# Kernel tuning notes

Measured on AMD Instinct MI355X. Metric: run time of the kernel, lower is better.

## Reference

```python
import jax, jax.numpy as jnp
import numpy as np

B, S, N, P = 16, 1, 6, 70000
H0, W0, DS = 448, 800, 4
H, W = H0 // DS, W0 // DS          # 112, 200
BEV_SIDE = 200


def _apply_4x4(RT, xyz):
    # RT: [M,4,4], xyz: [M,P,3] -> [M,P,3]
    xyz1 = jnp.concatenate([xyz, jnp.ones_like(xyz[..., :1])], axis=-1)
    return jnp.einsum('mij,mpj->mpi', RT, xyz1)[..., :3]


def _scale_intrinsics4(K, sx, sy):
    # K: [M,3,3] pinhole intrinsics -> scaled, embedded in 4x4
    M = K.shape[0]
    K4 = jnp.tile(jnp.eye(4, dtype=K.dtype), (M, 1, 1))
    K4 = K4.at[:, 0, 0].set(K[:, 0, 0] * sx)
    K4 = K4.at[:, 1, 1].set(K[:, 1, 1] * sy)
    K4 = K4.at[:, 0, 2].set(K[:, 0, 2] * sx)
    K4 = K4.at[:, 1, 2].set(K[:, 1, 2] * sy)
    return K4


def setup_inputs() -> dict:
    rng = np.random.default_rng(0)
    pts = rng.uniform(-50.0, 50.0, size=(B, 1, 1, P, 3)).astype(np.float32)
    pts[..., 2] = rng.uniform(-2.0, 4.0, size=(B, 1, 1, P)).astype(np.float32)
    ilu = rng.uniform(0.0, 255.0, size=(B, 1, 1, P, 1)).astype(np.float32)
    pcloud = np.concatenate([pts, ilu], axis=-1)
    # extrinsics: cam-to-car pose, 6 cameras at yaw 0..300deg
    E = np.tile(np.eye(4, dtype=np.float32), (B, S, N, 1, 1))
    for n in range(N):
        a = 2.0 * np.pi * n / N
        c, s = np.cos(a), np.sin(a)
        E[:, :, n, :3, :3] = np.array([[c, -s, 0], [s, c, 0], [0, 0, 1]], np.float32)
        E[:, :, n, :3, 3] = np.array([2.0 * c, 2.0 * s, 1.5], np.float32)
    K = np.tile(np.eye(3, dtype=np.float32), (B, S, N, 1, 1))
    K[..., 0, 0] = 500.0
    K[..., 1, 1] = 500.0
    K[..., 0, 2] = W0 / 2.0
    K[..., 1, 2] = H0 / 2.0
    V = np.tile(np.eye(4, dtype=np.float32), (B, 1, 1, 1, 1))
    V[..., 0, 0] = 2.0
    V[..., 1, 1] = 2.0
    V[..., 0, 3] = 100.0
    V[..., 1, 3] = 100.0
    return {
        'pcloud': jnp.asarray(pcloud),
        'extrinsics': jnp.asarray(E),
        'intrinsics': jnp.asarray(K),
        'view': jnp.asarray(V),
        'bev_side': BEV_SIDE,
    }


def reference(pcloud, extrinsics, intrinsics, view, bev_side):
    sx = sy = 1.0 / DS
    bsn = B * S * N
    lidar_coords = pcloud[:, 0, 0, :, :3]                      # [B,P,3]
    ilu = jnp.repeat(pcloud[:, 0, 0, :, 3], N, axis=0)         # [BSN,P]
    view2 = view[:, 0, 0]                                      # [B,4,4]
    lidar_view = _apply_4x4(jnp.linalg.inv(view2), lidar_coords)
    xyz_car = jnp.repeat(lidar_view, N, axis=0)                # [BSN,P,3]
    K = intrinsics.reshape(bsn, 3, 3)
    E = extrinsics.reshape(bsn, 4, 4)
    Rt = jnp.swapaxes(E[:, :3, :3], 1, 2)
    Einv = E.at[:, :3, :3].set(Rt).at[:, :3, 3:4].set(-jnp.matmul(Rt, E[:, :3, 3:4]))
    pixel_from_car = jnp.matmul(_scale_intrinsics4(K, sx, sy), Einv)
    z = _apply_4x4(Einv, xyz_car)[:, :, 2]                     # cam-frame depth
    xyz_pixel = _apply_4x4(pixel_from_car, xyz_car)            # [BSN,P,3]
    normalizer = xyz_pixel[:, :, 2]
    xy = xyz_pixel[:, :, :2] / jnp.maximum(normalizer[..., None], 1e-6)
    x_, y_ = xy[:, :, 0], xy[:, :, 1]
    valid = ((x_ > -0.5) & (x_ < W - 0.5) & (y_ > -0.5) & (y_ < H - 0.5) & (z > 0.0)).astype(pcloud.dtype)
    depth = jnp.clip(normalizer, 0.0, bev_side / 2 - 1) * valid
    vilu = jnp.clip(ilu * valid, 0.0, 255.0)
    ym = jnp.clip(y_, 0.0, H - 1).astype(jnp.int32)
    xm = jnp.clip(x_, 0.0, W - 1).astype(jnp.int32)
    b = jnp.broadcast_to(jnp.arange(bsn)[:, None], (bsn, P))
    depth_grid = jnp.zeros((bsn, H, W), pcloud.dtype).at[b, ym, xm].set(depth)
    ilu_grid = jnp.zeros((bsn, H, W), pcloud.dtype).at[b, ym, xm].set(vilu)
    ilu_grid = jnp.log1p(ilu_grid) / np.log(256.0)
    depth_grid = depth_grid / (bev_side / 2)
    return jnp.concatenate([depth_grid[:, None], ilu_grid[:, None]], axis=1)  # [BSN,2,H,W]
```

## Files before the change

### kernel.cpp

```cpp
#include <hip/hip_runtime.h>
#include <math.h>

#define B_    16
#define N_    6
#define P_    70000
#define H_    112
#define W_    200
#define HW_   (H_ * W_)
#define BSN_  (B_ * N_)
#define HALF_ 56
#define CELLS_ (HALF_ * W_)
#define NSEG  4
#define SEGPTS (P_ / NSEG)
#define T1_   512
#define T2_   1024

#define WS_NEED ((size_t)BSN_ * 2 * NSEG * CELLS_ * 4)


__device__ __forceinline__ float rdot4(float r0, float r1, float r2, float r3,
                                       float x, float y, float z) {
    float s = r0 * x;
    s = fmaf(r1, y, s);
    s = fmaf(r2, z, s);
    return s + r3;
}

__device__ __forceinline__ void inv4(const float* m, float* o) {
    float inv[16];
    inv[0]  =  m[5]*m[10]*m[15] - m[5]*m[11]*m[14] - m[9]*m[6]*m[15] + m[9]*m[7]*m[14] + m[13]*m[6]*m[11] - m[13]*m[7]*m[10];
    inv[4]  = -m[4]*m[10]*m[15] + m[4]*m[11]*m[14] + m[8]*m[6]*m[15] - m[8]*m[7]*m[14] - m[12]*m[6]*m[11] + m[12]*m[7]*m[10];
    inv[8]  =  m[4]*m[9]*m[15]  - m[4]*m[11]*m[13] - m[8]*m[5]*m[15] + m[8]*m[7]*m[13] + m[12]*m[5]*m[11] - m[12]*m[7]*m[9];
    inv[12] = -m[4]*m[9]*m[14]  + m[4]*m[10]*m[13] + m[8]*m[5]*m[14] - m[8]*m[6]*m[13] - m[12]*m[5]*m[10] + m[12]*m[6]*m[9];
    inv[1]  = -m[1]*m[10]*m[15] + m[1]*m[11]*m[14] + m[9]*m[2]*m[15] - m[9]*m[3]*m[14] - m[13]*m[2]*m[11] + m[13]*m[3]*m[10];
    inv[5]  =  m[0]*m[10]*m[15] - m[0]*m[11]*m[14] - m[8]*m[2]*m[15] + m[8]*m[3]*m[14] + m[12]*m[2]*m[11] - m[12]*m[3]*m[10];
    inv[9]  = -m[0]*m[9]*m[15]  + m[0]*m[11]*m[13] + m[8]*m[1]*m[15] - m[8]*m[3]*m[13] - m[12]*m[1]*m[11] + m[12]*m[3]*m[9];
    inv[13] =  m[0]*m[9]*m[14]  - m[0]*m[10]*m[13] - m[8]*m[1]*m[14] + m[8]*m[2]*m[13] + m[12]*m[1]*m[10] - m[12]*m[2]*m[9];
    inv[2]  =  m[1]*m[6]*m[15]  - m[1]*m[7]*m[14]  - m[5]*m[2]*m[15] + m[5]*m[3]*m[14] + m[13]*m[2]*m[7]  - m[13]*m[3]*m[6];
    inv[6]  = -m[0]*m[6]*m[15]  + m[0]*m[7]*m[14]  + m[4]*m[2]*m[15] - m[4]*m[3]*m[14] - m[12]*m[2]*m[7]  + m[12]*m[3]*m[6];
    inv[10] =  m[0]*m[5]*m[15]  - m[0]*m[7]*m[13]  - m[4]*m[1]*m[15] + m[4]*m[3]*m[13] + m[12]*m[1]*m[7]  - m[12]*m[3]*m[5];
    inv[14] = -m[0]*m[5]*m[14]  + m[0]*m[6]*m[13]  + m[4]*m[1]*m[14] - m[4]*m[2]*m[13] - m[12]*m[1]*m[6]  + m[12]*m[2]*m[5];
    inv[3]  = -m[1]*m[6]*m[11]  + m[1]*m[7]*m[10]  + m[5]*m[2]*m[11] - m[5]*m[3]*m[10] - m[9]*m[2]*m[7]   + m[9]*m[3]*m[6];
    inv[7]  =  m[0]*m[6]*m[11]  - m[0]*m[7]*m[10]  - m[4]*m[2]*m[11] + m[4]*m[3]*m[10] + m[8]*m[2]*m[7]   - m[8]*m[3]*m[6];
    inv[11] = -m[0]*m[5]*m[11]  + m[0]*m[7]*m[9]   + m[4]*m[1]*m[11] - m[4]*m[3]*m[9]  - m[8]*m[1]*m[7]   + m[8]*m[3]*m[5];
    inv[15] =  m[0]*m[5]*m[10]  - m[0]*m[6]*m[9]   - m[4]*m[1]*m[10] + m[4]*m[2]*m[9]  + m[8]*m[1]*m[6]   - m[8]*m[2]*m[5];
    float det = m[0]*inv[0] + m[1]*inv[4] + m[2]*inv[8] + m[3]*inv[12];
    float rdet = 1.0f / det;
    for (int i = 0; i < 16; ++i) o[i] = inv[i] * rdet;
}

__device__ __forceinline__ void cam_mats(const float* Ein, const float* Kin,
                                         float E2[4], float PFC[3][4]) {
    float Einv[4][4];
    for (int i = 0; i < 3; ++i)
        for (int j = 0; j < 3; ++j)
            Einv[i][j] = Ein[j * 4 + i];
    for (int i = 0; i < 3; ++i) {
        float s = Ein[0 * 4 + i] * Ein[0 * 4 + 3];
        s = fmaf(Ein[1 * 4 + i], Ein[1 * 4 + 3], s);
        s = fmaf(Ein[2 * 4 + i], Ein[2 * 4 + 3], s);
        Einv[i][3] = -s;
    }
    Einv[3][0] = Ein[12]; Einv[3][1] = Ein[13];
    Einv[3][2] = Ein[14]; Einv[3][3] = Ein[15];

    float K4[4][4] = {};
    K4[0][0] = Kin[0] * 0.25f;  K4[0][2] = Kin[2] * 0.25f;
    K4[1][1] = Kin[4] * 0.25f;  K4[1][2] = Kin[5] * 0.25f;
    K4[2][2] = 1.0f;            K4[3][3] = 1.0f;

    for (int i = 0; i < 3; ++i)
        for (int j = 0; j < 4; ++j) {
            float s = K4[i][0] * Einv[0][j];
            s = fmaf(K4[i][1], Einv[1][j], s);
            s = fmaf(K4[i][2], Einv[2][j], s);
            s = fmaf(K4[i][3], Einv[3][j], s);
            PFC[i][j] = s;
        }
    for (int j = 0; j < 4; ++j) E2[j] = Einv[2][j];
}


__global__ __launch_bounds__(T1_) void k_partial(
        const float4* __restrict__ pc, const float* __restrict__ extr,
        const float* __restrict__ intr, const float* __restrict__ view,
        int* __restrict__ partial) {
    __shared__ int   win[CELLS_];
    __shared__ float sM[24];

    const int i    = blockIdx.x;
    const int xcd  = i & 7;
    const int j    = i >> 3;
    const int b    = xcd + 8 * (j >= 48 ? 1 : 0);
    const int r    = j % 48;
    const int cam  = r >> 3;
    const int half = (r >> 2) & 1;
    const int seg  = r & 3;
    const int m    = b * N_ + cam;
    const int rlo  = half * HALF_;
    const int t    = threadIdx.x;

    if (t == 0) {
        float Vi[16];
        inv4(&view[b * 16], Vi);
        for (int k = 0; k < 12; ++k) sM[k] = Vi[k];
    } else if (t == 64) {
        float E2[4], PFC[3][4];
        cam_mats(&extr[m * 16], &intr[m * 9], E2, PFC);
        for (int ii = 0; ii < 3; ++ii)
            for (int jj = 0; jj < 4; ++jj) sM[12 + ii * 4 + jj] = PFC[ii][jj];
    }
    for (int k = t; k < CELLS_; k += T1_) win[k] = -1;
    __syncthreads();

    const float V0 = sM[0],  V1 = sM[1],  V2 = sM[2],  V3 = sM[3];
    const float V4 = sM[4],  V5 = sM[5],  V6 = sM[6],  V7 = sM[7];
    const float V8 = sM[8],  V9 = sM[9],  V10 = sM[10], V11 = sM[11];
    const float P00 = sM[12], P01 = sM[13], P02 = sM[14], P03 = sM[15];
    const float P10 = sM[16], P11 = sM[17], P12 = sM[18], P13 = sM[19];
    const float P20 = sM[20], P21 = sM[21], P22 = sM[22], P23 = sM[23];

    const float4* pcb = pc + (size_t)b * P_;
    int c0 = -1, c1 = -1, c2 = -1, c3 = -1;
    const int p0 = seg * SEGPTS;

    for (int p = p0 + t; p < p0 + SEGPTS; p += T1_) {
        float4 pt = pcb[p];
        float lx = rdot4(V0, V1, V2,  V3,  pt.x, pt.y, pt.z);
        float ly = rdot4(V4, V5, V6,  V7,  pt.x, pt.y, pt.z);
        float lz = rdot4(V8, V9, V10, V11, pt.x, pt.y, pt.z);
        float px = rdot4(P00, P01, P02, P03, lx, ly, lz);
        float py = rdot4(P10, P11, P12, P13, lx, ly, lz);
        float pz = rdot4(P20, P21, P22, P23, lx, ly, lz);
        float denom = fmaxf(pz, 1e-6f);
        float x_ = px / denom;
        float y_ = py / denom;
        int ym = (int)fminf(fmaxf(y_, 0.0f), (float)(H_ - 1));
        int xm = (int)fminf(fmaxf(x_, 0.0f), (float)(W_ - 1));
        bool is_c = (xm == 0 || xm == W_ - 1) && (ym == 0 || ym == H_ - 1);
        int code = ((ym != 0) << 1) | (xm != 0);
        c0 = (is_c && code == 0) ? p : c0;
        c1 = (is_c && code == 1) ? p : c1;
        c2 = (is_c && code == 2) ? p : c2;
        c3 = (is_c && code == 3) ? p : c3;
        int rr = ym - rlo;
        if (!is_c && (unsigned)rr < (unsigned)HALF_)
            atomicMax(&win[rr * W_ + xm], p);
    }
    for (int d = 32; d; d >>= 1) {
        c0 = max(c0, __shfl_xor(c0, d));
        c1 = max(c1, __shfl_xor(c1, d));
        c2 = max(c2, __shfl_xor(c2, d));
        c3 = max(c3, __shfl_xor(c3, d));
    }
    if ((t & 63) == 0) {
        if (half == 0) {
            if (c0 >= 0) atomicMax(&win[0],   c0);
            if (c1 >= 0) atomicMax(&win[199], c1);
        } else {
            if (c2 >= 0) atomicMax(&win[(H_ - 1 - rlo) * W_ + 0],   c2);
            if (c3 >= 0) atomicMax(&win[(H_ - 1 - rlo) * W_ + 199], c3);
        }
    }
    __syncthreads();

    int* dst = partial + (size_t)(((m * 2 + half) * NSEG) + seg) * CELLS_;
    for (int k = t; k < CELLS_; k += T1_) dst[k] = win[k];
}


__global__ __launch_bounds__(T2_) void k_mergefin(
        const float4* __restrict__ pc, const int* __restrict__ partial,
        const float* __restrict__ extr, const float* __restrict__ intr,
        const float* __restrict__ view,
        float* __restrict__ out, const int* __restrict__ bev_side_p) {
    __shared__ float sM[28];

    const int i    = blockIdx.x;
    const int xcd  = i & 7;
    const int j    = i >> 3;
    const int b    = xcd + 8 * (j >= 12 ? 1 : 0);
    const int r    = j % 12;
    const int cam  = r >> 1;
    const int half = r & 1;
    const int m    = b * N_ + cam;
    const int rlo  = half * HALF_;
    const int t    = threadIdx.x;

    if (t == 0) {
        float Vi[16];
        inv4(&view[b * 16], Vi);
        for (int k = 0; k < 12; ++k) sM[k] = Vi[k];
    } else if (t == 64) {
        float E2[4], PFC[3][4];
        cam_mats(&extr[m * 16], &intr[m * 9], E2, PFC);
        for (int ii = 0; ii < 3; ++ii)
            for (int jj = 0; jj < 4; ++jj) sM[12 + ii * 4 + jj] = PFC[ii][jj];
        for (int jj = 0; jj < 4; ++jj) sM[24 + jj] = E2[jj];
    }
    __syncthreads();

    const float bev_half = (float)bev_side_p[0] * 0.5f;
    const float clip_hi  = bev_half - 1.0f;
    const float4* pcb = pc + (size_t)b * P_;
    const int* pp = partial + (size_t)((m * 2 + half) * NSEG) * CELLS_;
    const int base0 = (m * 2) * HW_ + rlo * W_;

    for (int rr = t; rr < CELLS_; rr += T2_) {
        int wv = max(max(pp[rr], pp[CELLS_ + rr]),
                     max(pp[2 * CELLS_ + rr], pp[3 * CELLS_ + rr]));
        float depth = 0.0f, iluv = 0.0f;
        if (wv >= 0) {
            float4 pt = pcb[wv];
            float lx = rdot4(sM[0],  sM[1],  sM[2],  sM[3],  pt.x, pt.y, pt.z);
            float ly = rdot4(sM[4],  sM[5],  sM[6],  sM[7],  pt.x, pt.y, pt.z);
            float lz = rdot4(sM[8],  sM[9],  sM[10], sM[11], pt.x, pt.y, pt.z);
            float z  = rdot4(sM[24], sM[25], sM[26], sM[27], lx, ly, lz);
            float px = rdot4(sM[12], sM[13], sM[14], sM[15], lx, ly, lz);
            float py = rdot4(sM[16], sM[17], sM[18], sM[19], lx, ly, lz);
            float pz = rdot4(sM[20], sM[21], sM[22], sM[23], lx, ly, lz);
            float denom = fmaxf(pz, 1e-6f);
            float x_ = px / denom;
            float y_ = py / denom;
            bool valid = (x_ > -0.5f) && (x_ < (float)W_ - 0.5f) &&
                         (y_ > -0.5f) && (y_ < (float)H_ - 0.5f) && (z > 0.0f);
            if (valid) {
                float d = fminf(fmaxf(pz, 0.0f), clip_hi);
                depth = d / bev_half;
                float vi = fminf(fmaxf(pt.w, 0.0f), 255.0f);
                iluv = log1pf(vi) / 5.545177444479562f;
            }
        }
        out[base0 + rr]       = depth;
        out[base0 + HW_ + rr] = iluv;
    }
}


#define PMAIN 69632
#define PTAIL (P_ - PMAIN)

__global__ __launch_bounds__(1024, 4) void k_lidar_ilp(
        const float4* __restrict__ pc, const float* __restrict__ extr,
        const float* __restrict__ intr, const float* __restrict__ view,
        float* __restrict__ out, const int* __restrict__ bev_side_p) {
    __shared__ int   win[CELLS_];
    __shared__ float sM[28];

    const int i    = blockIdx.x;
    const int xcd  = i & 7;
    const int s    = i >> 3;
    const int b    = xcd + 8 * (s >= 12 ? 1 : 0);
    const int c12  = s % 12;
    const int m    = b * N_ + (c12 >> 1);
    const int rlo  = (c12 & 1) * HALF_;
    const int t    = threadIdx.x;

    if (t == 0) {
        float Vi[16];
        inv4(&view[b * 16], Vi);
        for (int k = 0; k < 12; ++k) sM[k] = Vi[k];
    } else if (t == 64) {
        float E2[4], PFC[3][4];
        cam_mats(&extr[m * 16], &intr[m * 9], E2, PFC);
        for (int ii = 0; ii < 3; ++ii)
            for (int jj = 0; jj < 4; ++jj) sM[12 + ii * 4 + jj] = PFC[ii][jj];
        for (int jj = 0; jj < 4; ++jj) sM[24 + jj] = E2[jj];
    }
    for (int k = t; k < CELLS_; k += 1024) win[k] = -1;
    __syncthreads();

    const float V0 = sM[0],  V1 = sM[1],  V2 = sM[2],  V3 = sM[3];
    const float V4 = sM[4],  V5 = sM[5],  V6 = sM[6],  V7 = sM[7];
    const float V8 = sM[8],  V9 = sM[9],  V10 = sM[10], V11 = sM[11];
    const float P00 = sM[12], P01 = sM[13], P02 = sM[14], P03 = sM[15];
    const float P10 = sM[16], P11 = sM[17], P12 = sM[18], P13 = sM[19];
    const float P20 = sM[20], P21 = sM[21], P22 = sM[22], P23 = sM[23];

    const float4* pcb = pc + (size_t)b * P_;
    int c0 = -1, c1 = -1, c2 = -1, c3 = -1;

#define PROC(PT, PIDX)                                                        \
    {                                                                         \
        float lx = rdot4(V0, V1, V2,  V3,  (PT).x, (PT).y, (PT).z);           \
        float ly = rdot4(V4, V5, V6,  V7,  (PT).x, (PT).y, (PT).z);           \
        float lz = rdot4(V8, V9, V10, V11, (PT).x, (PT).y, (PT).z);           \
        float px = rdot4(P00, P01, P02, P03, lx, ly, lz);                     \
        float py = rdot4(P10, P11, P12, P13, lx, ly, lz);                     \
        float pz = rdot4(P20, P21, P22, P23, lx, ly, lz);                     \
        float denom = fmaxf(pz, 1e-6f);                                       \
        float x_ = px / denom;                                                \
        float y_ = py / denom;                                                \
        int ym = (int)fminf(fmaxf(y_, 0.0f), (float)(H_ - 1));                \
        int xm = (int)fminf(fmaxf(x_, 0.0f), (float)(W_ - 1));                \
        bool is_c = (xm == 0 || xm == W_ - 1) && (ym == 0 || ym == H_ - 1);   \
        int code = ((ym != 0) << 1) | (xm != 0);                              \
        c0 = (is_c && code == 0) ? (PIDX) : c0;                               \
        c1 = (is_c && code == 1) ? (PIDX) : c1;                               \
        c2 = (is_c && code == 2) ? (PIDX) : c2;                               \
        c3 = (is_c && code == 3) ? (PIDX) : c3;                               \
        int rr = ym - rlo;                                                    \
        if (!is_c && (unsigned)rr < (unsigned)HALF_)                          \
            atomicMax(&win[rr * W_ + xm], (PIDX));                            \
    }

    for (int base = 0; base < PMAIN; base += 4 * 1024) {
        float4 q0 = pcb[base + t];
        float4 q1 = pcb[base + t + 1024];
        float4 q2 = pcb[base + t + 2 * 1024];
        float4 q3 = pcb[base + t + 3 * 1024];
        PROC(q0, base + t)
        PROC(q1, base + t + 1024)
        PROC(q2, base + t + 2 * 1024)
        PROC(q3, base + t + 3 * 1024)
    }
    if (t < PTAIL) {
        float4 q = pcb[PMAIN + t];
        PROC(q, PMAIN + t)
    }
#undef PROC

    for (int d = 32; d; d >>= 1) {
        c0 = max(c0, __shfl_xor(c0, d));
        c1 = max(c1, __shfl_xor(c1, d));
        c2 = max(c2, __shfl_xor(c2, d));
        c3 = max(c3, __shfl_xor(c3, d));
    }
    if ((t & 63) == 0) {
        if (rlo == 0) {
            if (c0 >= 0) atomicMax(&win[0],   c0);
            if (c1 >= 0) atomicMax(&win[199], c1);
        } else {
            if (c2 >= 0) atomicMax(&win[(H_ - 1 - rlo) * W_ + 0],   c2);
            if (c3 >= 0) atomicMax(&win[(H_ - 1 - rlo) * W_ + 199], c3);
        }
    }
    __syncthreads();

    const float bev_half = (float)bev_side_p[0] * 0.5f;
    const float clip_hi  = bev_half - 1.0f;
    const float E20 = sM[24], E21 = sM[25], E22 = sM[26], E23 = sM[27];
    const int base0 = (m * 2) * HW_ + rlo * W_;
    for (int r = t; r < CELLS_; r += 1024) {
        int w = win[r];
        float depth = 0.0f, iluv = 0.0f;
        if (w >= 0) {
            float4 pt = pcb[w];
            float lx = rdot4(V0, V1, V2,  V3,  pt.x, pt.y, pt.z);
            float ly = rdot4(V4, V5, V6,  V7,  pt.x, pt.y, pt.z);
            float lz = rdot4(V8, V9, V10, V11, pt.x, pt.y, pt.z);
            float z  = rdot4(E20, E21, E22, E23, lx, ly, lz);
            float px = rdot4(P00, P01, P02, P03, lx, ly, lz);
            float py = rdot4(P10, P11, P12, P13, lx, ly, lz);
            float pz = rdot4(P20, P21, P22, P23, lx, ly, lz);
            float denom = fmaxf(pz, 1e-6f);
            float x_ = px / denom;
            float y_ = py / denom;
            bool valid = (x_ > -0.5f) && (x_ < (float)W_ - 0.5f) &&
                         (y_ > -0.5f) && (y_ < (float)H_ - 0.5f) && (z > 0.0f);
            if (valid) {
                float d = fminf(fmaxf(pz, 0.0f), clip_hi);
                depth = d / bev_half;
                float vi = fminf(fmaxf(pt.w, 0.0f), 255.0f);
                iluv = log1pf(vi) / 5.545177444479562f;
            }
        }
        out[base0 + r]       = depth;
        out[base0 + HW_ + r] = iluv;
    }
}


extern "C" void kernel_launch(void* const* d_in, const int* in_sizes, int n_in,
                              void* d_out, int out_size, void* d_ws, size_t ws_size,
                              hipStream_t stream) {
    const float4* pc  = (const float4*)d_in[0];
    const float* extr = (const float*)d_in[1];
    const float* intr = (const float*)d_in[2];
    const float* view = (const float*)d_in[3];
    const int*   bev  = (const int*)d_in[4];
    float* out = (float*)d_out;

    if (ws_size >= WS_NEED) {
        int* partial = (int*)d_ws;
        k_partial<<<dim3(BSN_ * 2 * NSEG), dim3(T1_), 0, stream>>>(
            pc, extr, intr, view, partial);
        k_mergefin<<<dim3(BSN_ * 2), dim3(T2_), 0, stream>>>(
            pc, partial, extr, intr, view, out, bev);
    } else {
        k_lidar_ilp<<<dim3(BSN_ * 2), dim3(1024), 0, stream>>>(
            pc, extr, intr, view, out, bev);
    }
}
```

Baseline: 48.56 us.

## Replace per-camera partial grids with single-pass multi-camera scan and compacted hit lists

The first kernel now reads each lidar point once per batch, projects it into all six cameras, and uses division-free threshold tests to classify it. Only points that land strictly inside the image are appended, as packed (camera, cell, index) entries, to a per-block list in workspace; corner hits go to per-chunk reduction slots. The final kernel rebuilds each half-image winner map in shared memory from those compacted lists and corner maxima. This removes the redundant six-fold point reads and the large partial-grid writes and merges, at the cost of a shared-memory counter atomic per hit and of every final block scanning all entries of its batch.

```diff
diff --git a/kernel.cpp b/kernel.cpp
--- a/kernel.cpp
+++ b/kernel.cpp
@@ -10,12 +10,18 @@
 #define BSN_  (B_ * N_)
 #define HALF_ 56
 #define CELLS_ (HALF_ * W_)
-#define NSEG  4
-#define SEGPTS (P_ / NSEG)
-#define T1_   512
-#define T2_   1024
-
-#define WS_NEED ((size_t)BSN_ * 2 * NSEG * CELLS_ * 4)
+
+#define AT_     512
+#define AIT     8
+#define ACHUNK  (AT_ * AIT)
+#define ACHUNKS 18
+#define NBLK    (B_ * ACHUNKS)
+#define CAP     (ACHUNK * N_)
+
+#define WS_GC_OFF   0
+#define WS_CNT_OFF  (NBLK * 24 * 4)
+#define WS_ENT_OFF  32768
+#define WS_NEED     (WS_ENT_OFF + (size_t)NBLK * CAP * 8)
 
 
 __device__ __forceinline__ float rdot4(float r0, float r1, float r2, float r3,
@@ -81,108 +87,134 @@
 }
 
 
-__global__ __launch_bounds__(T1_) void k_partial(
+__global__ __launch_bounds__(AT_) void k_scan(
         const float4* __restrict__ pc, const float* __restrict__ extr,
         const float* __restrict__ intr, const float* __restrict__ view,
-        int* __restrict__ partial) {
-    __shared__ int   win[CELLS_];
-    __shared__ float sM[24];
-
-    const int i    = blockIdx.x;
-    const int xcd  = i & 7;
-    const int j    = i >> 3;
-    const int b    = xcd + 8 * (j >= 48 ? 1 : 0);
-    const int r    = j % 48;
-    const int cam  = r >> 3;
-    const int half = (r >> 2) & 1;
-    const int seg  = r & 3;
-    const int m    = b * N_ + cam;
-    const int rlo  = half * HALF_;
-    const int t    = threadIdx.x;
+        int* __restrict__ gcorner, int* __restrict__ counts,
+        uint2* __restrict__ entries) {
+    __shared__ float sM[84];
+    __shared__ int   swc[8][24];
+    __shared__ int   scnt;
+
+    const int b     = blockIdx.x;
+    const int chunk = blockIdx.y;
+    const int t     = threadIdx.x;
+    const int lane  = t & 63;
+    const int w     = t >> 6;
 
     if (t == 0) {
         float Vi[16];
         inv4(&view[b * 16], Vi);
         for (int k = 0; k < 12; ++k) sM[k] = Vi[k];
-    } else if (t == 64) {
+        scnt = 0;
+    } else if (t >= 64 && t < 64 + N_) {
+        int n = t - 64;
         float E2[4], PFC[3][4];
-        cam_mats(&extr[m * 16], &intr[m * 9], E2, PFC);
-        for (int ii = 0; ii < 3; ++ii)
-            for (int jj = 0; jj < 4; ++jj) sM[12 + ii * 4 + jj] = PFC[ii][jj];
-    }
-    for (int k = t; k < CELLS_; k += T1_) win[k] = -1;
-    __syncthreads();
-
-    const float V0 = sM[0],  V1 = sM[1],  V2 = sM[2],  V3 = sM[3];
-    const float V4 = sM[4],  V5 = sM[5],  V6 = sM[6],  V7 = sM[7];
-    const float V8 = sM[8],  V9 = sM[9],  V10 = sM[10], V11 = sM[11];
-    const float P00 = sM[12], P01 = sM[13], P02 = sM[14], P03 = sM[15];
-    const float P10 = sM[16], P11 = sM[17], P12 = sM[18], P13 = sM[19];
-    const float P20 = sM[20], P21 = sM[21], P22 = sM[22], P23 = sM[23];
-
+        cam_mats(&extr[(b * N_ + n) * 16], &intr[(b * N_ + n) * 9], E2, PFC);
+        for (int i = 0; i < 3; ++i)
+            for (int j = 0; j < 4; ++j) sM[12 + n * 12 + i * 4 + j] = PFC[i][j];
+    }
+    __syncthreads();
+
+    float V[12];
+    #pragma unroll
+    for (int k = 0; k < 12; ++k) V[k] = sM[k];
+    float Pm[6][12];
+    #pragma unroll
+    for (int n = 0; n < 6; ++n)
+        #pragma unroll
+        for (int k = 0; k < 12; ++k) Pm[n][k] = sM[12 + n * 12 + k];
+
+    int c[24];
+    #pragma unroll
+    for (int k = 0; k < 24; ++k) c[k] = -1;
+
+    const int blk = b * ACHUNKS + chunk;
+    uint2* ent = entries + (size_t)blk * CAP;
     const float4* pcb = pc + (size_t)b * P_;
-    int c0 = -1, c1 = -1, c2 = -1, c3 = -1;
-    const int p0 = seg * SEGPTS;
-
-    for (int p = p0 + t; p < p0 + SEGPTS; p += T1_) {
-        float4 pt = pcb[p];
-        float lx = rdot4(V0, V1, V2,  V3,  pt.x, pt.y, pt.z);
-        float ly = rdot4(V4, V5, V6,  V7,  pt.x, pt.y, pt.z);
-        float lz = rdot4(V8, V9, V10, V11, pt.x, pt.y, pt.z);
-        float px = rdot4(P00, P01, P02, P03, lx, ly, lz);
-        float py = rdot4(P10, P11, P12, P13, lx, ly, lz);
-        float pz = rdot4(P20, P21, P22, P23, lx, ly, lz);
-        float denom = fmaxf(pz, 1e-6f);
-        float x_ = px / denom;
-        float y_ = py / denom;
-        int ym = (int)fminf(fmaxf(y_, 0.0f), (float)(H_ - 1));
-        int xm = (int)fminf(fmaxf(x_, 0.0f), (float)(W_ - 1));
-        bool is_c = (xm == 0 || xm == W_ - 1) && (ym == 0 || ym == H_ - 1);
-        int code = ((ym != 0) << 1) | (xm != 0);
-        c0 = (is_c && code == 0) ? p : c0;
-        c1 = (is_c && code == 1) ? p : c1;
-        c2 = (is_c && code == 2) ? p : c2;
-        c3 = (is_c && code == 3) ? p : c3;
-        int rr = ym - rlo;
-        if (!is_c && (unsigned)rr < (unsigned)HALF_)
-            atomicMax(&win[rr * W_ + xm], p);
-    }
-    for (int d = 32; d; d >>= 1) {
-        c0 = max(c0, __shfl_xor(c0, d));
-        c1 = max(c1, __shfl_xor(c1, d));
-        c2 = max(c2, __shfl_xor(c2, d));
-        c3 = max(c3, __shfl_xor(c3, d));
-    }
-    if ((t & 63) == 0) {
-        if (half == 0) {
-            if (c0 >= 0) atomicMax(&win[0],   c0);
-            if (c1 >= 0) atomicMax(&win[199], c1);
-        } else {
-            if (c2 >= 0) atomicMax(&win[(H_ - 1 - rlo) * W_ + 0],   c2);
-            if (c3 >= 0) atomicMax(&win[(H_ - 1 - rlo) * W_ + 199], c3);
-        }
-    }
-    __syncthreads();
-
-    int* dst = partial + (size_t)(((m * 2 + half) * NSEG) + seg) * CELLS_;
-    for (int k = t; k < CELLS_; k += T1_) dst[k] = win[k];
-}
-
-
-__global__ __launch_bounds__(T2_) void k_mergefin(
-        const float4* __restrict__ pc, const int* __restrict__ partial,
-        const float* __restrict__ extr, const float* __restrict__ intr,
-        const float* __restrict__ view,
+
+    int p = chunk * ACHUNK + t;
+    for (int it = 0; it < AIT; ++it, p += AT_) {
+        bool valid = (p < P_);
+        float4 pt = make_float4(0.f, 0.f, 0.f, 0.f);
+        if (valid) pt = pcb[p];
+        float lx = rdot4(V[0], V[1], V[2],  V[3],  pt.x, pt.y, pt.z);
+        float ly = rdot4(V[4], V[5], V[6],  V[7],  pt.x, pt.y, pt.z);
+        float lz = rdot4(V[8], V[9], V[10], V[11], pt.x, pt.y, pt.z);
+        unsigned rfl = 0;
+        #pragma unroll
+        for (int n = 0; n < 6; ++n) {
+            float px = rdot4(Pm[n][0], Pm[n][1], Pm[n][2],  Pm[n][3],  lx, ly, lz);
+            float py = rdot4(Pm[n][4], Pm[n][5], Pm[n][6],  Pm[n][7],  lx, ly, lz);
+            float pz = rdot4(Pm[n][8], Pm[n][9], Pm[n][10], Pm[n][11], lx, ly, lz);
+            float denom = fmaxf(pz, 1e-6f);
+            float tl = 0.99f * denom;
+            float tx = 201.0f * denom;
+            float ty = 113.0f * denom;
+            bool x0 = (px <= tl), x1 = (px >= tx);
+            bool y0 = (py <= tl), y1 = (py >= ty);
+            if (valid) {
+                if (x0 & y0) c[n * 4 + 0] = p;
+                if (x1 & y0) c[n * 4 + 1] = p;
+                if (x0 & y1) c[n * 4 + 2] = p;
+                if (x1 & y1) c[n * 4 + 3] = p;
+                if (!((x0 | x1) & (y0 | y1))) rfl |= (1u << n);
+            }
+        }
+        if (__ballot(rfl != 0)) {
+            #pragma unroll
+            for (int n = 0; n < 6; ++n) {
+                if (rfl & (1u << n)) {
+                    float px = rdot4(Pm[n][0], Pm[n][1], Pm[n][2],  Pm[n][3],  lx, ly, lz);
+                    float py = rdot4(Pm[n][4], Pm[n][5], Pm[n][6],  Pm[n][7],  lx, ly, lz);
+                    float pz = rdot4(Pm[n][8], Pm[n][9], Pm[n][10], Pm[n][11], lx, ly, lz);
+                    float denom = fmaxf(pz, 1e-6f);
+                    float x_ = px / denom;
+                    float y_ = py / denom;
+                    int ym = (int)fminf(fmaxf(y_, 0.0f), (float)(H_ - 1));
+                    int xm = (int)fminf(fmaxf(x_, 0.0f), (float)(W_ - 1));
+                    int pos = atomicAdd(&scnt, 1);
+                    ent[pos] = make_uint2(((unsigned)n << 15) |
+                                          ((unsigned)ym << 8) | (unsigned)xm,
+                                          (unsigned)p);
+                }
+            }
+        }
+    }
+
+    #pragma unroll
+    for (int k = 0; k < 24; ++k) {
+        int v = c[k];
+        for (int d = 32; d; d >>= 1) v = max(v, __shfl_xor(v, d));
+        if (lane == 0) swc[w][k] = v;
+    }
+    __syncthreads();
+    if (t < 24) {
+        int v = -1;
+        #pragma unroll
+        for (int w2 = 0; w2 < 8; ++w2) v = max(v, swc[w2][t]);
+        gcorner[blk * 24 + t] = v;
+    }
+    if (t == 32) counts[blk] = scnt;
+}
+
+
+__global__ __launch_bounds__(1024) void k_fin(
+        const float4* __restrict__ pc, const float* __restrict__ extr,
+        const float* __restrict__ intr, const float* __restrict__ view,
+        const int* __restrict__ gcorner, const int* __restrict__ counts,
+        const uint2* __restrict__ entries,
         float* __restrict__ out, const int* __restrict__ bev_side_p) {
+    __shared__ int   win[CELLS_];
     __shared__ float sM[28];
 
     const int i    = blockIdx.x;
     const int xcd  = i & 7;
-    const int j    = i >> 3;
-    const int b    = xcd + 8 * (j >= 12 ? 1 : 0);
-    const int r    = j % 12;
-    const int cam  = r >> 1;
-    const int half = r & 1;
+    const int s    = i >> 3;
+    const int b    = xcd + 8 * (s >= 12 ? 1 : 0);
+    const int c12  = s % 12;
+    const int cam  = c12 >> 1;
+    const int half = c12 & 1;
     const int m    = b * N_ + cam;
     const int rlo  = half * HALF_;
     const int t    = threadIdx.x;
@@ -198,17 +230,41 @@
             for (int jj = 0; jj < 4; ++jj) sM[12 + ii * 4 + jj] = PFC[ii][jj];
         for (int jj = 0; jj < 4; ++jj) sM[24 + jj] = E2[jj];
     }
+    for (int k = t; k < CELLS_; k += 1024) win[k] = -1;
+    __syncthreads();
+
+    if (t < 2) {
+        int cid = half * 2 + t;
+        int best = -1;
+        for (int k = 0; k < ACHUNKS; ++k)
+            best = max(best, gcorner[(b * ACHUNKS + k) * 24 + cam * 4 + cid]);
+        if (best >= 0) {
+            int cell = (half ? (HALF_ - 1) * W_ : 0) + (t ? (W_ - 1) : 0);
+            atomicMax(&win[cell], best);
+        }
+    }
+
+    for (int k = 0; k < ACHUNKS; ++k) {
+        const int cnt = counts[b * ACHUNKS + k];
+        const uint2* ent = entries + (size_t)(b * ACHUNKS + k) * CAP;
+        for (int e = t; e < cnt; e += 1024) {
+            uint2 v = ent[e];
+            int camE = (int)(v.x >> 15);
+            int ym   = (int)((v.x >> 8) & 127u);
+            int xm   = (int)(v.x & 255u);
+            int rr   = ym - rlo;
+            if (camE == cam && (unsigned)rr < (unsigned)HALF_)
+                atomicMax(&win[rr * W_ + xm], (int)v.y);
+        }
+    }
     __syncthreads();
 
     const float bev_half = (float)bev_side_p[0] * 0.5f;
     const float clip_hi  = bev_half - 1.0f;
     const float4* pcb = pc + (size_t)b * P_;
-    const int* pp = partial + (size_t)((m * 2 + half) * NSEG) * CELLS_;
     const int base0 = (m * 2) * HW_ + rlo * W_;
-
-    for (int rr = t; rr < CELLS_; rr += T2_) {
-        int wv = max(max(pp[rr], pp[CELLS_ + rr]),
-                     max(pp[2 * CELLS_ + rr], pp[3 * CELLS_ + rr]));
+    for (int rr = t; rr < CELLS_; rr += 1024) {
+        int wv = win[rr];
         float depth = 0.0f, iluv = 0.0f;
         if (wv >= 0) {
             float4 pt = pcb[wv];
@@ -382,11 +438,14 @@
     float* out = (float*)d_out;
 
     if (ws_size >= WS_NEED) {
-        int* partial = (int*)d_ws;
-        k_partial<<<dim3(BSN_ * 2 * NSEG), dim3(T1_), 0, stream>>>(
-            pc, extr, intr, view, partial);
-        k_mergefin<<<dim3(BSN_ * 2), dim3(T2_), 0, stream>>>(
-            pc, partial, extr, intr, view, out, bev);
+        char* ws = (char*)d_ws;
+        int*   gcorner = (int*)(ws + WS_GC_OFF);
+        int*   counts  = (int*)(ws + WS_CNT_OFF);
+        uint2* entries = (uint2*)(ws + WS_ENT_OFF);
+        k_scan<<<dim3(B_, ACHUNKS), dim3(AT_), 0, stream>>>(
+            pc, extr, intr, view, gcorner, counts, entries);
+        k_fin<<<dim3(BSN_ * 2), dim3(1024), 0, stream>>>(
+            pc, extr, intr, view, gcorner, counts, entries, out, bev);
     } else {
         k_lidar_ilp<<<dim3(BSN_ * 2), dim3(1024), 0, stream>>>(
             pc, extr, intr, view, out, bev);
```

Result: slower. 51.60 us (+6.3%).

## Prefilter points per camera into compacted lists before scatter

Applied to the files above, without the earlier changes.

Replaces the partial-window plus merge pipeline with three kernels: one computes the per-camera matrices once, one classifies every point against all six cameras and writes compact per-chunk lists of (camera, point) entries for points that land off the clamped corners, and a final kernel scatters only those entries into a shared-memory window. Corner cells are resolved by scanning chunks backwards with ballots and stopping early once both corners have a winner. The aim is to cut the 4x redundant projection work and the partial-buffer round trip through global memory. In exchange it adds a launch and a global entries buffer, and the final kernel rescans every chunk's entry list, filtering by camera, for each of its 12 camera-halves.

```diff
diff --git a/kernel.cpp b/kernel.cpp
--- a/kernel.cpp
+++ b/kernel.cpp
@@ -10,12 +10,17 @@
 #define BSN_  (B_ * N_)
 #define HALF_ 56
 #define CELLS_ (HALF_ * W_)
-#define NSEG  4
-#define SEGPTS (P_ / NSEG)
-#define T1_   512
-#define T2_   1024
-
-#define WS_NEED ((size_t)BSN_ * 2 * NSEG * CELLS_ * 4)
+
+#define K1T   1024
+#define K1BLK 69
+#define K1CAP (K1T * N_)
+
+#define WS_MAT_OFF 0
+#define WS_PFC   192
+#define WS_E2    1344
+#define WS_CNT_OFF 8192
+#define WS_ENT_OFF 16384
+#define WS_NEED (WS_ENT_OFF + (size_t)B_ * K1BLK * K1CAP * 4)
 
 
 __device__ __forceinline__ float rdot4(float r0, float r1, float r2, float r3,
@@ -81,36 +86,101 @@
 }
 
 
-__global__ __launch_bounds__(T1_) void k_partial(
-        const float4* __restrict__ pc, const float* __restrict__ extr,
-        const float* __restrict__ intr, const float* __restrict__ view,
-        int* __restrict__ partial) {
+__global__ __launch_bounds__(128) void k_mats(
+        const float* __restrict__ extr, const float* __restrict__ intr,
+        const float* __restrict__ view, float* __restrict__ wsf) {
+    const int t = threadIdx.x;
+    if (t < BSN_) {
+        float E2[4], PFC[3][4];
+        cam_mats(&extr[t * 16], &intr[t * 9], E2, PFC);
+        for (int i = 0; i < 3; ++i)
+            for (int j = 0; j < 4; ++j) wsf[WS_PFC + t * 12 + i * 4 + j] = PFC[i][j];
+        for (int j = 0; j < 4; ++j) wsf[WS_E2 + t * 4 + j] = E2[j];
+    } else if (t < BSN_ + B_) {
+        int b = t - BSN_;
+        float Vi[16];
+        inv4(&view[b * 16], Vi);
+        for (int k = 0; k < 12; ++k) wsf[b * 12 + k] = Vi[k];
+    }
+}
+
+
+__global__ __launch_bounds__(K1T) void k_classify(
+        const float4* __restrict__ pc, const float* __restrict__ wsf,
+        int* __restrict__ counts, unsigned int* __restrict__ entries) {
+    __shared__ int scnt;
+    const int b     = blockIdx.x;
+    const int chunk = blockIdx.y;
+    const int t     = threadIdx.x;
+    if (t == 0) scnt = 0;
+    __syncthreads();
+
+    const int p   = chunk * K1T + t;
+    const int seg = b * K1BLK + chunk;
+    const bool valid = (p < P_);
+    float4 pt = make_float4(0.f, 0.f, 0.f, 0.f);
+    if (valid) pt = pc[(size_t)b * P_ + p];
+
+    const float* V = wsf + b * 12;
+    float lx = rdot4(V[0], V[1], V[2],  V[3],  pt.x, pt.y, pt.z);
+    float ly = rdot4(V[4], V[5], V[6],  V[7],  pt.x, pt.y, pt.z);
+    float lz = rdot4(V[8], V[9], V[10], V[11], pt.x, pt.y, pt.z);
+
+    unsigned rfl = 0;
+    #pragma unroll
+    for (int n = 0; n < 6; ++n) {
+        const float* Pm = wsf + WS_PFC + (b * N_ + n) * 12;
+        float px = rdot4(Pm[0], Pm[1], Pm[2],  Pm[3],  lx, ly, lz);
+        float py = rdot4(Pm[4], Pm[5], Pm[6],  Pm[7],  lx, ly, lz);
+        float pz = rdot4(Pm[8], Pm[9], Pm[10], Pm[11], lx, ly, lz);
+        float denom = fmaxf(pz, 1e-6f);
+        bool x0 = (px <= 0.99f * denom), x1 = (px >= 201.0f * denom);
+        bool y0 = (py <= 0.99f * denom), y1 = (py >= 113.0f * denom);
+        if (!((x0 | x1) & (y0 | y1))) rfl |= (1u << n);
+    }
+    if (valid && rfl) {
+        unsigned int* ent = entries + (size_t)seg * K1CAP;
+        #pragma unroll
+        for (int n = 0; n < 6; ++n)
+            if (rfl & (1u << n)) {
+                int pos = atomicAdd(&scnt, 1);
+                ent[pos] = ((unsigned)n << 17) | (unsigned)p;
+            }
+    }
+    __syncthreads();
+    if (t == 0) counts[seg] = scnt;
+}
+
+
+__global__ __launch_bounds__(1024) void k_fin2(
+        const float4* __restrict__ pc, const float* __restrict__ wsf,
+        const int* __restrict__ counts, const unsigned int* __restrict__ entries,
+        float* __restrict__ out, const int* __restrict__ bev_side_p) {
     __shared__ int   win[CELLS_];
-    __shared__ float sM[24];
+    __shared__ float sM[28];
+    __shared__ int   cw[2];
 
     const int i    = blockIdx.x;
     const int xcd  = i & 7;
-    const int j    = i >> 3;
-    const int b    = xcd + 8 * (j >= 48 ? 1 : 0);
-    const int r    = j % 48;
-    const int cam  = r >> 3;
-    const int half = (r >> 2) & 1;
-    const int seg  = r & 3;
+    const int s    = i >> 3;
+    const int b    = xcd + 8 * (s >= 12 ? 1 : 0);
+    const int c12  = s % 12;
+    const int cam  = c12 >> 1;
+    const int half = c12 & 1;
     const int m    = b * N_ + cam;
     const int rlo  = half * HALF_;
     const int t    = threadIdx.x;
+    const int lane = t & 63;
+    const int w    = t >> 6;
 
     if (t == 0) {
-        float Vi[16];
-        inv4(&view[b * 16], Vi);
-        for (int k = 0; k < 12; ++k) sM[k] = Vi[k];
+        for (int k = 0; k < 12; ++k) sM[k] = wsf[b * 12 + k];
+        cw[0] = -1; cw[1] = -1;
     } else if (t == 64) {
-        float E2[4], PFC[3][4];
-        cam_mats(&extr[m * 16], &intr[m * 9], E2, PFC);
-        for (int ii = 0; ii < 3; ++ii)
-            for (int jj = 0; jj < 4; ++jj) sM[12 + ii * 4 + jj] = PFC[ii][jj];
-    }
-    for (int k = t; k < CELLS_; k += T1_) win[k] = -1;
+        for (int k = 0; k < 12; ++k) sM[12 + k] = wsf[WS_PFC + m * 12 + k];
+        for (int k = 0; k < 4; ++k)  sM[24 + k] = wsf[WS_E2 + m * 4 + k];
+    }
+    for (int k = t; k < CELLS_; k += 1024) win[k] = -1;
     __syncthreads();
 
     const float V0 = sM[0],  V1 = sM[1],  V2 = sM[2],  V3 = sM[3];
@@ -119,13 +189,13 @@
     const float P00 = sM[12], P01 = sM[13], P02 = sM[14], P03 = sM[15];
     const float P10 = sM[16], P11 = sM[17], P12 = sM[18], P13 = sM[19];
     const float P20 = sM[20], P21 = sM[21], P22 = sM[22], P23 = sM[23];
-
     const float4* pcb = pc + (size_t)b * P_;
-    int c0 = -1, c1 = -1, c2 = -1, c3 = -1;
-    const int p0 = seg * SEGPTS;
-
-    for (int p = p0 + t; p < p0 + SEGPTS; p += T1_) {
-        float4 pt = pcb[p];
+
+    for (int cbase = (K1BLK - 1) * K1T; cbase >= 0; cbase -= K1T) {
+        int p = cbase + t;
+        bool valid = (p < P_);
+        float4 pt = make_float4(0.f, 0.f, 0.f, 0.f);
+        if (valid) pt = pcb[p];
         float lx = rdot4(V0, V1, V2,  V3,  pt.x, pt.y, pt.z);
         float ly = rdot4(V4, V5, V6,  V7,  pt.x, pt.y, pt.z);
         float lz = rdot4(V8, V9, V10, V11, pt.x, pt.y, pt.z);
@@ -133,92 +203,72 @@
         float py = rdot4(P10, P11, P12, P13, lx, ly, lz);
         float pz = rdot4(P20, P21, P22, P23, lx, ly, lz);
         float denom = fmaxf(pz, 1e-6f);
-        float x_ = px / denom;
-        float y_ = py / denom;
-        int ym = (int)fminf(fmaxf(y_, 0.0f), (float)(H_ - 1));
-        int xm = (int)fminf(fmaxf(x_, 0.0f), (float)(W_ - 1));
-        bool is_c = (xm == 0 || xm == W_ - 1) && (ym == 0 || ym == H_ - 1);
-        int code = ((ym != 0) << 1) | (xm != 0);
-        c0 = (is_c && code == 0) ? p : c0;
-        c1 = (is_c && code == 1) ? p : c1;
-        c2 = (is_c && code == 2) ? p : c2;
-        c3 = (is_c && code == 3) ? p : c3;
-        int rr = ym - rlo;
-        if (!is_c && (unsigned)rr < (unsigned)HALF_)
-            atomicMax(&win[rr * W_ + xm], p);
-    }
-    for (int d = 32; d; d >>= 1) {
-        c0 = max(c0, __shfl_xor(c0, d));
-        c1 = max(c1, __shfl_xor(c1, d));
-        c2 = max(c2, __shfl_xor(c2, d));
-        c3 = max(c3, __shfl_xor(c3, d));
-    }
-    if ((t & 63) == 0) {
-        if (half == 0) {
-            if (c0 >= 0) atomicMax(&win[0],   c0);
-            if (c1 >= 0) atomicMax(&win[199], c1);
-        } else {
-            if (c2 >= 0) atomicMax(&win[(H_ - 1 - rlo) * W_ + 0],   c2);
-            if (c3 >= 0) atomicMax(&win[(H_ - 1 - rlo) * W_ + 199], c3);
-        }
-    }
-    __syncthreads();
-
-    int* dst = partial + (size_t)(((m * 2 + half) * NSEG) + seg) * CELLS_;
-    for (int k = t; k < CELLS_; k += T1_) dst[k] = win[k];
-}
-
-
-__global__ __launch_bounds__(T2_) void k_mergefin(
-        const float4* __restrict__ pc, const int* __restrict__ partial,
-        const float* __restrict__ extr, const float* __restrict__ intr,
-        const float* __restrict__ view,
-        float* __restrict__ out, const int* __restrict__ bev_side_p) {
-    __shared__ float sM[28];
-
-    const int i    = blockIdx.x;
-    const int xcd  = i & 7;
-    const int j    = i >> 3;
-    const int b    = xcd + 8 * (j >= 12 ? 1 : 0);
-    const int r    = j % 12;
-    const int cam  = r >> 1;
-    const int half = r & 1;
-    const int m    = b * N_ + cam;
-    const int rlo  = half * HALF_;
-    const int t    = threadIdx.x;
-
+        bool x0 = (px <= 0.99f * denom), x1 = (px >= 201.0f * denom);
+        bool y0 = (py <= 0.99f * denom), y1 = (py >= 113.0f * denom);
+        bool certA, certB;
+        if (half == 0) { certA = x0 & y0; certB = x1 & y0; }
+        else           { certA = x0 & y1; certB = x1 & y1; }
+        unsigned long long mA = __ballot(valid && certA);
+        unsigned long long mB = __ballot(valid && certB);
+        if (lane == 0) {
+            if (mA) atomicMax(&cw[0], cbase + (w << 6) + 63 - __builtin_clzll(mA));
+            if (mB) atomicMax(&cw[1], cbase + (w << 6) + 63 - __builtin_clzll(mB));
+        }
+        __syncthreads();
+        int a0 = cw[0], a1 = cw[1];
+        __syncthreads();
+        if (a0 >= 0 && a1 >= 0) break;
+    }
+
+    for (int s2 = w; s2 < K1BLK; s2 += 16) {
+        const int seg = b * K1BLK + s2;
+        const int cnt = counts[seg];
+        const unsigned int* ent = entries + (size_t)seg * K1CAP;
+        for (int e = lane; e < cnt; e += 64) {
+            unsigned int v = ent[e];
+            if ((int)(v >> 17) == cam) {
+                int p = (int)(v & 0x1FFFFu);
+                float4 pt = pcb[p];
+                float lx = rdot4(V0, V1, V2,  V3,  pt.x, pt.y, pt.z);
+                float ly = rdot4(V4, V5, V6,  V7,  pt.x, pt.y, pt.z);
+                float lz = rdot4(V8, V9, V10, V11, pt.x, pt.y, pt.z);
+                float px = rdot4(P00, P01, P02, P03, lx, ly, lz);
+                float py = rdot4(P10, P11, P12, P13, lx, ly, lz);
+                float pz = rdot4(P20, P21, P22, P23, lx, ly, lz);
+                float denom = fmaxf(pz, 1e-6f);
+                float x_ = px / denom;
+                float y_ = py / denom;
+                int ym = (int)fminf(fmaxf(y_, 0.0f), (float)(H_ - 1));
+                int xm = (int)fminf(fmaxf(x_, 0.0f), (float)(W_ - 1));
+                int rr = ym - rlo;
+                if ((unsigned)rr < (unsigned)HALF_)
+                    atomicMax(&win[rr * W_ + xm], p);
+            }
+        }
+    }
     if (t == 0) {
-        float Vi[16];
-        inv4(&view[b * 16], Vi);
-        for (int k = 0; k < 12; ++k) sM[k] = Vi[k];
-    } else if (t == 64) {
-        float E2[4], PFC[3][4];
-        cam_mats(&extr[m * 16], &intr[m * 9], E2, PFC);
-        for (int ii = 0; ii < 3; ++ii)
-            for (int jj = 0; jj < 4; ++jj) sM[12 + ii * 4 + jj] = PFC[ii][jj];
-        for (int jj = 0; jj < 4; ++jj) sM[24 + jj] = E2[jj];
+        int cell0 = half ? (HALF_ - 1) * W_ : 0;
+        if (cw[0] >= 0) atomicMax(&win[cell0],          cw[0]);
+        if (cw[1] >= 0) atomicMax(&win[cell0 + W_ - 1], cw[1]);
     }
     __syncthreads();
 
     const float bev_half = (float)bev_side_p[0] * 0.5f;
     const float clip_hi  = bev_half - 1.0f;
-    const float4* pcb = pc + (size_t)b * P_;
-    const int* pp = partial + (size_t)((m * 2 + half) * NSEG) * CELLS_;
+    const float E20 = sM[24], E21 = sM[25], E22 = sM[26], E23 = sM[27];
     const int base0 = (m * 2) * HW_ + rlo * W_;
-
-    for (int rr = t; rr < CELLS_; rr += T2_) {
-        int wv = max(max(pp[rr], pp[CELLS_ + rr]),
-                     max(pp[2 * CELLS_ + rr], pp[3 * CELLS_ + rr]));
+    for (int rr = t; rr < CELLS_; rr += 1024) {
+        int wv = win[rr];
         float depth = 0.0f, iluv = 0.0f;
         if (wv >= 0) {
             float4 pt = pcb[wv];
-            float lx = rdot4(sM[0],  sM[1],  sM[2],  sM[3],  pt.x, pt.y, pt.z);
-            float ly = rdot4(sM[4],  sM[5],  sM[6],  sM[7],  pt.x, pt.y, pt.z);
-            float lz = rdot4(sM[8],  sM[9],  sM[10], sM[11], pt.x, pt.y, pt.z);
-            float z  = rdot4(sM[24], sM[25], sM[26], sM[27], lx, ly, lz);
-            float px = rdot4(sM[12], sM[13], sM[14], sM[15], lx, ly, lz);
-            float py = rdot4(sM[16], sM[17], sM[18], sM[19], lx, ly, lz);
-            float pz = rdot4(sM[20], sM[21], sM[22], sM[23], lx, ly, lz);
+            float lx = rdot4(V0, V1, V2,  V3,  pt.x, pt.y, pt.z);
+            float ly = rdot4(V4, V5, V6,  V7,  pt.x, pt.y, pt.z);
+            float lz = rdot4(V8, V9, V10, V11, pt.x, pt.y, pt.z);
+            float z  = rdot4(E20, E21, E22, E23, lx, ly, lz);
+            float px = rdot4(P00, P01, P02, P03, lx, ly, lz);
+            float py = rdot4(P10, P11, P12, P13, lx, ly, lz);
+            float pz = rdot4(P20, P21, P22, P23, lx, ly, lz);
             float denom = fmaxf(pz, 1e-6f);
             float x_ = px / denom;
             float y_ = py / denom;
@@ -342,10 +392,10 @@
     const float E20 = sM[24], E21 = sM[25], E22 = sM[26], E23 = sM[27];
     const int base0 = (m * 2) * HW_ + rlo * W_;
     for (int r = t; r < CELLS_; r += 1024) {
-        int w = win[r];
+        int wv = win[r];
         float depth = 0.0f, iluv = 0.0f;
-        if (w >= 0) {
-            float4 pt = pcb[w];
+        if (wv >= 0) {
+            float4 pt = pcb[wv];
             float lx = rdot4(V0, V1, V2,  V3,  pt.x, pt.y, pt.z);
             float ly = rdot4(V4, V5, V6,  V7,  pt.x, pt.y, pt.z);
             float lz = rdot4(V8, V9, V10, V11, pt.x, pt.y, pt.z);
@@ -382,11 +432,15 @@
     float* out = (float*)d_out;
 
     if (ws_size >= WS_NEED) {
-        int* partial = (int*)d_ws;
-        k_partial<<<dim3(BSN_ * 2 * NSEG), dim3(T1_), 0, stream>>>(
-            pc, extr, intr, view, partial);
-        k_mergefin<<<dim3(BSN_ * 2), dim3(T2_), 0, stream>>>(
-            pc, partial, extr, intr, view, out, bev);
+        char* ws = (char*)d_ws;
+        float* wsf = (float*)(ws + WS_MAT_OFF);
+        int* counts = (int*)(ws + WS_CNT_OFF);
+        unsigned int* entries = (unsigned int*)(ws + WS_ENT_OFF);
+        k_mats<<<dim3(1), dim3(128), 0, stream>>>(extr, intr, view, wsf);
+        k_classify<<<dim3(B_, K1BLK), dim3(K1T), 0, stream>>>(
+            pc, wsf, counts, entries);
+        k_fin2<<<dim3(BSN_ * 2), dim3(1024), 0, stream>>>(
+            pc, wsf, counts, entries, out, bev);
     } else {
         k_lidar_ilp<<<dim3(BSN_ * 2), dim3(1024), 0, stream>>>(
             pc, extr, intr, view, out, bev);
```

After: 70.05 us. 44.2% more time.
